# Kernel tuning notes

Hardware: AMD Instinct MI355X
Metric: run time of the kernel (lower is better)

Reference implementation:

```python
import jax, jax.numpy as jnp
import numpy as np

IN_DIM = 512
OUT_DIM = 512
KEY_DIM = 512
FILTER_LENGTH = 32
STRIDE = 4
B, T = 8, 2048


def setup_inputs() -> dict:
    key = jax.random.key(0)
    ks = jax.random.split(key, 7)
    s_in = 1.0 / np.sqrt(IN_DIM)
    x = jax.random.normal(ks[0], (B, T, IN_DIM), dtype=jnp.float32)
    Wq = jax.random.uniform(ks[1], (IN_DIM, KEY_DIM), jnp.float32, -s_in, s_in)
    bq = jax.random.uniform(ks[2], (KEY_DIM,), jnp.float32, -s_in, s_in)
    Wk = jax.random.uniform(ks[3], (IN_DIM, KEY_DIM), jnp.float32, -s_in, s_in)
    bk = jax.random.uniform(ks[4], (KEY_DIM,), jnp.float32, -s_in, s_in)
    Wv = jax.random.uniform(ks[5], (IN_DIM, OUT_DIM), jnp.float32, -s_in, s_in)
    bv = jax.random.uniform(ks[6], (OUT_DIM,), jnp.float32, -s_in, s_in)
    return {"x": x, "Wq": Wq, "bq": bq, "Wk": Wk, "bk": bk, "Wv": Wv, "bv": bv}


def reference(x, Wq, bq, Wk, bk, Wv, bv):
    # x: (B, T, in_dim)
    Bsz, T_, _ = x.shape
    F = FILTER_LENGTH
    T_out = (T_ - F) // STRIDE + 1
    starts = jnp.arange(T_out) * STRIDE                 # (T_out,)
    win_idx = starts[:, None] + jnp.arange(F)[None, :]  # (T_out, F)
    center_idx = starts + F // 2                        # (T_out,)

    q = x @ Wq + bq   # (B, T, key_dim)
    k = x @ Wk + bk   # (B, T, key_dim)
    v = x @ Wv + bv   # (B, T, out_dim)

    q_c = q[:, center_idx]    # (B, T_out, key_dim) query at window center
    k_w = k[:, win_idx]       # (B, T_out, F, key_dim)
    v_w = v[:, win_idx]       # (B, T_out, F, out_dim)

    scale = 1.0 / jnp.sqrt(jnp.asarray(KEY_DIM, dtype=q.dtype))
    scores = jnp.einsum('btd,btfd->btf', q_c, k_w) * scale  # (B, T_out, F)
    attn = jax.nn.softmax(scores, axis=-1)
    out = jnp.einsum('btf,btfd->btd', attn, v_w)            # (B, T_out, out_dim)
    return out
```

## Files before the change

### kernel.cpp

```cpp
#include <hip/hip_runtime.h>
#include <hip/hip_bf16.h>
#include <cstdint>

#define FLT 32
#define TOUT 505
#define TT 2048
#define MROWS 16384
#define QROWS 4040
#define KDIM 512
#define BK 64
#define NT 8

typedef float f32x4 __attribute__((ext_vector_type(4)));
typedef __bf16 bf16x8 __attribute__((ext_vector_type(8)));

static __device__ __forceinline__ ushort f2bf(float f) {
  uint32_t u = __float_as_uint(f);
  uint32_t r = (u + 0x7fffu + ((u >> 16) & 1u)) >> 16;
  return (ushort)r;
}
static __device__ __forceinline__ float bf2f(ushort h) {
  return __uint_as_float(((uint32_t)h) << 16);
}

__global__ void prep_kernel(const float* __restrict__ x,
                            const float* __restrict__ Wq, const float* __restrict__ Wk,
                            const float* __restrict__ Wv, const float* __restrict__ bq,
                            const float* __restrict__ bk, const float* __restrict__ bv,
                            ushort* __restrict__ xb, ushort* __restrict__ wt,
                            float* __restrict__ bias) {
  const int bid = blockIdx.x;
  const int tid = threadIdx.x;
  if (bid < 8192) {
    int i = bid * 256 + tid;
    float4 v = reinterpret_cast<const float4*>(x)[i];
    ushort4 o;
    o.x = f2bf(v.x); o.y = f2bf(v.y); o.z = f2bf(v.z); o.w = f2bf(v.w);
    reinterpret_cast<ushort4*>(xb)[i] = o;
  } else if (bid < 8384) {
    __shared__ ushort lds[64][66];
    int w = bid - 8192;
    int mat = w >> 6;
    int rem = w & 63;
    int k0 = (rem >> 3) * 64;
    int n0 = (rem & 7) * 64;
    const float* W = (mat == 0) ? Wq : (mat == 1) ? Wk : Wv;
    int nn = tid & 63;
    #pragma unroll
    for (int r = 0; r < 16; ++r) {
      int kk = r * 4 + (tid >> 6);
      lds[kk][nn] = f2bf(W[(size_t)(k0 + kk) * 512 + n0 + nn]);
    }
    __syncthreads();
    int kk2 = tid & 63;
    #pragma unroll
    for (int r = 0; r < 16; ++r) {
      int nn2 = r * 4 + (tid >> 6);
      wt[(size_t)(mat * 512 + n0 + nn2) * 512 + k0 + kk2] = lds[kk2][nn2];
    }
  } else {
    #pragma unroll
    for (int e = 0; e < 6; ++e) {
      int n = tid * 6 + e;
      const float* bsrc = (n < 512) ? bq : (n < 1024) ? bk : bv;
      bias[n] = bsrc[n & 511];
    }
  }
}

__global__ __launch_bounds__(256, 2) void gemm_kernel(
    const ushort* __restrict__ xb, const ushort* __restrict__ wt,
    const float* __restrict__ bias, ushort* __restrict__ kv, ushort* __restrict__ qc) {
  __shared__ ushort As[128 * 64];
  __shared__ ushort Bs[128 * 64];

  const int tid = threadIdx.x;
  const int lane = tid & 63;
  const int wv = tid >> 6;
  const int bid = blockIdx.x;

  int m0, n0, ost, gather;
  const ushort* wtb;
  const float* biasb;
  ushort* outp;
  if (bid < 1024) {
    int swz = (bid & 7) * 128 + (bid >> 3);
    m0 = (swz >> 3) * 128; n0 = (swz & 7) * 128;
    wtb = wt + (size_t)512 * KDIM; biasb = bias + 512;
    outp = kv; ost = 1024; gather = 0;
  } else {
    int b2 = bid - 1024;
    int swz = (b2 & 7) * 16 + (b2 >> 3);
    m0 = (swz >> 2) * 128; n0 = (swz & 3) * 128;
    wtb = wt; biasb = bias;
    outp = qc; ost = 512; gather = 1;
  }

  const ushort* aSrc[4];
  const ushort* bSrc[4];
  #pragma unroll
  for (int i = 0; i < 4; ++i) {
    int boff = i * 4096 + wv * 1024 + lane * 16;
    int row = boff >> 7;
    int colb = boff & 127;
    int scol = (colb ^ ((row & 7) << 4)) >> 1;
    size_t arow;
    if (gather) {
      int r = m0 + row;
      if (r > QROWS - 1) r = QROWS - 1;
      int bb = r / TOUT;
      int t2 = r - bb * TOUT;
      arow = (size_t)bb * TT + (size_t)t2 * 4 + FLT / 2;
    } else {
      arow = (size_t)(m0 + row);
    }
    aSrc[i] = xb + arow * KDIM + scol;
    bSrc[i] = wtb + (size_t)(n0 + row) * KDIM + scol;
  }

  const int fr = lane & 15;
  const int fq = lane >> 4;
  const int wr = wv >> 1;
  const int wc = wv & 1;

  f32x4 acc[4][4];
  #pragma unroll
  for (int i = 0; i < 4; ++i)
    #pragma unroll
    for (int j = 0; j < 4; ++j) acc[i][j] = (f32x4){0.f, 0.f, 0.f, 0.f};

  for (int t = 0; t < NT; ++t) {
    __syncthreads();
    const int koff = t * BK;
    #pragma unroll
    for (int i = 0; i < 4; ++i) {
      int ldst = i * 4096 + wv * 1024 + lane * 16;
      __builtin_amdgcn_global_load_lds(
          (const __attribute__((address_space(1))) unsigned int*)(aSrc[i] + koff),
          (__attribute__((address_space(3))) unsigned int*)((char*)As + ldst),
          16, 0, 0);
      __builtin_amdgcn_global_load_lds(
          (const __attribute__((address_space(1))) unsigned int*)(bSrc[i] + koff),
          (__attribute__((address_space(3))) unsigned int*)((char*)Bs + ldst),
          16, 0, 0);
    }
    __syncthreads();

    #pragma unroll
    for (int ks = 0; ks < 2; ++ks) {
      bf16x8 af[4], bg[4];
      #pragma unroll
      for (int i = 0; i < 4; ++i) {
        int ra = wr * 64 + i * 16 + fr;
        int ca = ks * 64 + fq * 16;
        af[i] = *reinterpret_cast<const bf16x8*>(
            (const char*)As + ra * 128 + (ca ^ ((ra & 7) << 4)));
        int rb = wc * 64 + i * 16 + fr;
        bg[i] = *reinterpret_cast<const bf16x8*>(
            (const char*)Bs + rb * 128 + (ca ^ ((rb & 7) << 4)));
      }
      #pragma unroll
      for (int i = 0; i < 4; ++i)
        #pragma unroll
        for (int j = 0; j < 4; ++j)
          acc[i][j] = __builtin_amdgcn_mfma_f32_16x16x32_bf16(af[i], bg[j], acc[i][j], 0, 0, 0);
    }
  }

  #pragma unroll
  for (int j = 0; j < 4; ++j) {
    int col = n0 + wc * 64 + j * 16 + fr;
    float bvl = biasb[col];
    #pragma unroll
    for (int i = 0; i < 4; ++i) {
      int rowb = m0 + wr * 64 + i * 16 + fq * 4;
      #pragma unroll
      for (int r = 0; r < 4; ++r) {
        if (!gather || (rowb + r) < QROWS)
          outp[(size_t)(rowb + r) * ost + col] = f2bf(acc[i][j][r] + bvl);
      }
    }
  }
}

__global__ __launch_bounds__(256) void attn_kernel(
    const ushort* __restrict__ kv,
    const ushort* __restrict__ qc,
    float* __restrict__ out) {
  __shared__ float q_lds[KDIM];
  __shared__ float s_lds[FLT];
  __shared__ float p_lds[FLT];

  const int bid = blockIdx.x;
  const int b = bid & 7;
  const int t = bid >> 3;
  const size_t base_row = (size_t)b * TT + (size_t)t * 4;
  const int tid = threadIdx.x;
  const int lane = tid & 63;
  const int wv = tid >> 6;

  {
    const ushort* qrow = qc + ((size_t)b * TOUT + t) * KDIM;
    uint v = *reinterpret_cast<const uint*>(qrow + tid * 2);
    q_lds[tid * 2]     = bf2f((ushort)(v & 0xffffu));
    q_lds[tid * 2 + 1] = bf2f((ushort)(v >> 16));
  }
  __syncthreads();

  const int fl = lane >> 3;
  const int f = wv * 8 + fl;
  const int sub = lane & 7;
  const ushort* krow = kv + (base_row + f) * 1024;
  float acc = 0.f;
  #pragma unroll
  for (int j = 0; j < 8; ++j) {
    int d = (j * 8 + sub) * 8;
    uint4 kv4 = *reinterpret_cast<const uint4*>(krow + d);
    const ushort* ks = reinterpret_cast<const ushort*>(&kv4);
    #pragma unroll
    for (int e = 0; e < 8; ++e) acc += q_lds[d + e] * bf2f(ks[e]);
  }
  acc += __shfl_xor(acc, 1);
  acc += __shfl_xor(acc, 2);
  acc += __shfl_xor(acc, 4);
  if (sub == 0) s_lds[f] = acc * 0.04419417382415922f;
  __syncthreads();

  float m = -1e30f;
  #pragma unroll
  for (int i = 0; i < FLT; ++i) m = fmaxf(m, s_lds[i]);
  if (tid < FLT) p_lds[tid] = __expf(s_lds[tid] - m);
  __syncthreads();
  float sum = 0.f;
  #pragma unroll
  for (int i = 0; i < FLT; ++i) sum += p_lds[i];
  const float inv = 1.f / sum;

  const int d = tid * 2;
  float o0 = 0.f, o1 = 0.f;
  const ushort* vbase = kv + base_row * 1024 + 512 + d;
  #pragma unroll
  for (int ff = 0; ff < FLT; ++ff) {
    uint vvv = *reinterpret_cast<const uint*>(vbase + (size_t)ff * 1024);
    float w = p_lds[ff] * inv;
    o0 += w * bf2f((ushort)(vvv & 0xffffu));
    o1 += w * bf2f((ushort)(vvv >> 16));
  }
  float2* op = reinterpret_cast<float2*>(out + ((size_t)b * TOUT + t) * 512 + d);
  *op = make_float2(o0, o1);
}

extern "C" void kernel_launch(void* const* d_in, const int* in_sizes, int n_in,
                              void* d_out, int out_size, void* d_ws, size_t ws_size,
                              hipStream_t stream) {
  const float* x  = (const float*)d_in[0];
  const float* Wq = (const float*)d_in[1];
  const float* bq = (const float*)d_in[2];
  const float* Wk = (const float*)d_in[3];
  const float* bk = (const float*)d_in[4];
  const float* Wv = (const float*)d_in[5];
  const float* bv = (const float*)d_in[6];
  float* out = (float*)d_out;

  char* ws = (char*)d_ws;
  ushort* xb   = (ushort*)ws;
  ushort* wt   = (ushort*)(ws + 16777216);
  float*  bias = (float*)(ws + 16777216 + 1572864);
  ushort* kvb  = (ushort*)(ws + 18358272);
  ushort* qc   = (ushort*)(ws + 18358272 + 33554432);

  hipLaunchKernelGGL(prep_kernel, dim3(8385), dim3(256), 0, stream,
                     x, Wq, Wk, Wv, bq, bk, bv, xb, wt, bias);
  hipLaunchKernelGGL(gemm_kernel, dim3(1152), dim3(256), 0, stream,
                     xb, wt, bias, kvb, qc);
  hipLaunchKernelGGL(attn_kernel, dim3(QROWS), dim3(256), 0, stream, kvb, qc, out);
}
```

Measured before the change: 72.13 us.

## Reassociate attention to avoid computing K and V over all timesteps

Rather than projecting K and V for every input row, the query is projected only at window centres and then multiplied by Wk (z = q·Wkᵀ), so scores become z·x over raw x windows. The key bias term is constant across a window and cancels in the softmax. The attention-weighted sum of x is then projected through Wv, and bv is added at the end because the weights sum to one. This removes the large K/V GEMM over 16384 rows, but adds two small chained GEMMs, fp32 x windows staged in LDS (64KB per block), and an extra bf16 rounding of intermediates.

```diff
diff --git a/kernel.cpp b/kernel.cpp
--- a/kernel.cpp
+++ b/kernel.cpp
@@ -2,14 +2,12 @@
 #include <hip/hip_bf16.h>
 #include <cstdint>
 
-#define FLT 32
 #define TOUT 505
-#define TT 2048
-#define MROWS 16384
+#define TT   2048
 #define QROWS 4040
-#define KDIM 512
-#define BK 64
-#define NT 8
+#define KD   512
+#define BK   128
+#define NSTEP 4
 
 typedef float f32x4 __attribute__((ext_vector_type(4)));
 typedef __bf16 bf16x8 __attribute__((ext_vector_type(8)));
@@ -23,28 +21,19 @@
   return __uint_as_float(((uint32_t)h) << 16);
 }
 
-__global__ void prep_kernel(const float* __restrict__ x,
-                            const float* __restrict__ Wq, const float* __restrict__ Wk,
-                            const float* __restrict__ Wv, const float* __restrict__ bq,
-                            const float* __restrict__ bk, const float* __restrict__ bv,
-                            ushort* __restrict__ xb, ushort* __restrict__ wt,
-                            float* __restrict__ bias) {
+__global__ void prep_kernel(const float* __restrict__ Wq, const float* __restrict__ Wk,
+                            const float* __restrict__ Wv,
+                            ushort* __restrict__ wqt, ushort* __restrict__ wvt,
+                            ushort* __restrict__ wkb) {
   const int bid = blockIdx.x;
   const int tid = threadIdx.x;
-  if (bid < 8192) {
-    int i = bid * 256 + tid;
-    float4 v = reinterpret_cast<const float4*>(x)[i];
-    ushort4 o;
-    o.x = f2bf(v.x); o.y = f2bf(v.y); o.z = f2bf(v.z); o.w = f2bf(v.w);
-    reinterpret_cast<ushort4*>(xb)[i] = o;
-  } else if (bid < 8384) {
+  if (bid < 128) {
     __shared__ ushort lds[64][66];
-    int w = bid - 8192;
-    int mat = w >> 6;
-    int rem = w & 63;
-    int k0 = (rem >> 3) * 64;
-    int n0 = (rem & 7) * 64;
-    const float* W = (mat == 0) ? Wq : (mat == 1) ? Wk : Wv;
+    int mat = bid >> 6;
+    int w = bid & 63;
+    int k0 = (w >> 3) * 64, n0 = (w & 7) * 64;
+    const float* W = mat ? Wv : Wq;
+    ushort* dst = mat ? wvt : wqt;
     int nn = tid & 63;
     #pragma unroll
     for (int r = 0; r < 16; ++r) {
@@ -56,66 +45,57 @@
     #pragma unroll
     for (int r = 0; r < 16; ++r) {
       int nn2 = r * 4 + (tid >> 6);
-      wt[(size_t)(mat * 512 + n0 + nn2) * 512 + k0 + kk2] = lds[kk2][nn2];
+      dst[(size_t)(n0 + nn2) * 512 + k0 + kk2] = lds[kk2][nn2];
     }
   } else {
-    #pragma unroll
-    for (int e = 0; e < 6; ++e) {
-      int n = tid * 6 + e;
-      const float* bsrc = (n < 512) ? bq : (n < 1024) ? bk : bv;
-      bias[n] = bsrc[n & 511];
-    }
-  }
-}
-
+    int idx = (bid - 128) * 256 + tid;
+    int e0 = idx * 8;
+    float4 a = *reinterpret_cast<const float4*>(Wk + e0);
+    float4 b = *reinterpret_cast<const float4*>(Wk + e0 + 4);
+    ushort v8[8] = {f2bf(a.x), f2bf(a.y), f2bf(a.z), f2bf(a.w),
+                    f2bf(b.x), f2bf(b.y), f2bf(b.z), f2bf(b.w)};
+    *reinterpret_cast<uint4*>(wkb + e0) = *reinterpret_cast<const uint4*>(v8);
+  }
+}
+
+template <int MODE>
 __global__ __launch_bounds__(256, 2) void gemm_kernel(
-    const ushort* __restrict__ xb, const ushort* __restrict__ wt,
-    const float* __restrict__ bias, ushort* __restrict__ kv, ushort* __restrict__ qc) {
-  __shared__ ushort As[128 * 64];
-  __shared__ ushort Bs[128 * 64];
+    const float* __restrict__ xf, const ushort* __restrict__ abuf,
+    const ushort* __restrict__ bmat, const float* __restrict__ bias,
+    ushort* __restrict__ obf, float* __restrict__ of32) {
+  __shared__ ushort As[128 * 128];
+  __shared__ ushort Bs[128 * 128];
 
   const int tid = threadIdx.x;
   const int lane = tid & 63;
   const int wv = tid >> 6;
-  const int bid = blockIdx.x;
-
-  int m0, n0, ost, gather;
-  const ushort* wtb;
-  const float* biasb;
-  ushort* outp;
-  if (bid < 1024) {
-    int swz = (bid & 7) * 128 + (bid >> 3);
-    m0 = (swz >> 3) * 128; n0 = (swz & 7) * 128;
-    wtb = wt + (size_t)512 * KDIM; biasb = bias + 512;
-    outp = kv; ost = 1024; gather = 0;
-  } else {
-    int b2 = bid - 1024;
-    int swz = (b2 & 7) * 16 + (b2 >> 3);
-    m0 = (swz >> 2) * 128; n0 = (swz & 3) * 128;
-    wtb = wt; biasb = bias;
-    outp = qc; ost = 512; gather = 1;
-  }
-
-  const ushort* aSrc[4];
-  const ushort* bSrc[4];
-  #pragma unroll
-  for (int i = 0; i < 4; ++i) {
-    int boff = i * 4096 + wv * 1024 + lane * 16;
-    int row = boff >> 7;
-    int colb = boff & 127;
-    int scol = (colb ^ ((row & 7) << 4)) >> 1;
-    size_t arow;
-    if (gather) {
-      int r = m0 + row;
-      if (r > QROWS - 1) r = QROWS - 1;
+  const int swz = (blockIdx.x & 7) * 16 + (blockIdx.x >> 3);
+  const int m0 = (swz >> 2) * 128;
+  const int n0 = (swz & 3) * 128;
+
+  const int srow = tid >> 4;
+  const int colb = (tid & 15) * 16;
+  const int scol = ((((colb & 127) ^ ((srow & 7) << 4)) + (colb & 128)) >> 1);
+
+  const ushort* bSrc[8];
+  const ushort* aSrc[8];
+  const float*  aSrcF[8];
+  uint          aDst[8];
+  #pragma unroll
+  for (int i = 0; i < 8; ++i) {
+    int row = i * 16 + srow;
+    bSrc[i] = bmat + (size_t)(n0 + row) * 512 + scol;
+    if (MODE == 0) {
+      int r = m0 + row; if (r > QROWS - 1) r = QROWS - 1;
       int bb = r / TOUT;
-      int t2 = r - bb * TOUT;
-      arow = (size_t)bb * TT + (size_t)t2 * 4 + FLT / 2;
+      int tt = r - bb * TOUT;
+      size_t arow = (size_t)bb * TT + (size_t)tt * 4 + 16;
+      aSrcF[i] = xf + arow * 512 + (colb >> 1);
+      aDst[i] = (uint)(row * 256 + (colb & 128) + ((colb & 127) ^ ((row & 7) << 4)));
     } else {
-      arow = (size_t)(m0 + row);
-    }
-    aSrc[i] = xb + arow * KDIM + scol;
-    bSrc[i] = wtb + (size_t)(n0 + row) * KDIM + scol;
+      int r = m0 + row; if (r > QROWS - 1) r = QROWS - 1;
+      aSrc[i] = abuf + (size_t)r * 512 + scol;
+    }
   }
 
   const int fr = lane & 15;
@@ -129,35 +109,44 @@
     #pragma unroll
     for (int j = 0; j < 4; ++j) acc[i][j] = (f32x4){0.f, 0.f, 0.f, 0.f};
 
-  for (int t = 0; t < NT; ++t) {
+  for (int t = 0; t < NSTEP; ++t) {
     __syncthreads();
     const int koff = t * BK;
     #pragma unroll
-    for (int i = 0; i < 4; ++i) {
-      int ldst = i * 4096 + wv * 1024 + lane * 16;
-      __builtin_amdgcn_global_load_lds(
-          (const __attribute__((address_space(1))) unsigned int*)(aSrc[i] + koff),
-          (__attribute__((address_space(3))) unsigned int*)((char*)As + ldst),
-          16, 0, 0);
+    for (int i = 0; i < 8; ++i) {
+      int ldst = i * 4096 + tid * 16;
       __builtin_amdgcn_global_load_lds(
           (const __attribute__((address_space(1))) unsigned int*)(bSrc[i] + koff),
           (__attribute__((address_space(3))) unsigned int*)((char*)Bs + ldst),
           16, 0, 0);
+      if (MODE == 0) {
+        float4 lo = *reinterpret_cast<const float4*>(aSrcF[i] + koff);
+        float4 hi = *reinterpret_cast<const float4*>(aSrcF[i] + koff + 4);
+        ushort v8[8] = {f2bf(lo.x), f2bf(lo.y), f2bf(lo.z), f2bf(lo.w),
+                        f2bf(hi.x), f2bf(hi.y), f2bf(hi.z), f2bf(hi.w)};
+        *reinterpret_cast<uint4*>((char*)As + aDst[i]) =
+            *reinterpret_cast<const uint4*>(v8);
+      } else {
+        __builtin_amdgcn_global_load_lds(
+            (const __attribute__((address_space(1))) unsigned int*)(aSrc[i] + koff),
+            (__attribute__((address_space(3))) unsigned int*)((char*)As + ldst),
+            16, 0, 0);
+      }
     }
     __syncthreads();
 
     #pragma unroll
-    for (int ks = 0; ks < 2; ++ks) {
+    for (int ks = 0; ks < 4; ++ks) {
+      const int cab = ks * 64 + fq * 16;
       bf16x8 af[4], bg[4];
       #pragma unroll
       for (int i = 0; i < 4; ++i) {
         int ra = wr * 64 + i * 16 + fr;
-        int ca = ks * 64 + fq * 16;
         af[i] = *reinterpret_cast<const bf16x8*>(
-            (const char*)As + ra * 128 + (ca ^ ((ra & 7) << 4)));
+            (const char*)As + ra * 256 + (cab & 128) + ((cab & 127) ^ ((ra & 7) << 4)));
         int rb = wc * 64 + i * 16 + fr;
         bg[i] = *reinterpret_cast<const bf16x8*>(
-            (const char*)Bs + rb * 128 + (ca ^ ((rb & 7) << 4)));
+            (const char*)Bs + rb * 256 + (cab & 128) + ((cab & 127) ^ ((rb & 7) << 4)));
       }
       #pragma unroll
       for (int i = 0; i < 4; ++i)
@@ -170,55 +159,68 @@
   #pragma unroll
   for (int j = 0; j < 4; ++j) {
     int col = n0 + wc * 64 + j * 16 + fr;
-    float bvl = biasb[col];
+    float bvl = (MODE == 1) ? 0.f : bias[col];
     #pragma unroll
     for (int i = 0; i < 4; ++i) {
       int rowb = m0 + wr * 64 + i * 16 + fq * 4;
       #pragma unroll
       for (int r = 0; r < 4; ++r) {
-        if (!gather || (rowb + r) < QROWS)
-          outp[(size_t)(rowb + r) * ost + col] = f2bf(acc[i][j][r] + bvl);
+        if (rowb + r < QROWS) {
+          float v = acc[i][j][r] + bvl;
+          if (MODE == 2) of32[(size_t)(rowb + r) * 512 + col] = v;
+          else           obf[(size_t)(rowb + r) * 512 + col] = f2bf(v);
+        }
       }
     }
   }
 }
 
 __global__ __launch_bounds__(256) void attn_kernel(
-    const ushort* __restrict__ kv,
-    const ushort* __restrict__ qc,
-    float* __restrict__ out) {
-  __shared__ float q_lds[KDIM];
-  __shared__ float s_lds[FLT];
-  __shared__ float p_lds[FLT];
+    const float* __restrict__ xf,
+    const ushort* __restrict__ zbuf,
+    ushort* __restrict__ ubuf) {
+  __shared__ float xw[32 * 512];
+  __shared__ float zl[512];
+  __shared__ float s_lds[32];
+  __shared__ float p_lds[32];
 
   const int bid = blockIdx.x;
   const int b = bid & 7;
   const int t = bid >> 3;
   const size_t base_row = (size_t)b * TT + (size_t)t * 4;
+  const int r = b * TOUT + t;
   const int tid = threadIdx.x;
   const int lane = tid & 63;
   const int wv = tid >> 6;
 
+  #pragma unroll
+  for (int i = 0; i < 16; ++i) {
+    int dst = i * 4096 + tid * 16;
+    int row = dst >> 11;
+    int cf = (dst & 2047) >> 2;
+    __builtin_amdgcn_global_load_lds(
+        (const __attribute__((address_space(1))) unsigned int*)(xf + (base_row + row) * 512 + cf),
+        (__attribute__((address_space(3))) unsigned int*)((char*)xw + dst),
+        16, 0, 0);
+  }
   {
-    const ushort* qrow = qc + ((size_t)b * TOUT + t) * KDIM;
-    uint v = *reinterpret_cast<const uint*>(qrow + tid * 2);
-    q_lds[tid * 2]     = bf2f((ushort)(v & 0xffffu));
-    q_lds[tid * 2 + 1] = bf2f((ushort)(v >> 16));
+    uint v = *reinterpret_cast<const uint*>(zbuf + (size_t)r * 512 + tid * 2);
+    zl[tid * 2]     = bf2f((ushort)(v & 0xffffu));
+    zl[tid * 2 + 1] = bf2f((ushort)(v >> 16));
   }
   __syncthreads();
 
-  const int fl = lane >> 3;
-  const int f = wv * 8 + fl;
+  const int f = wv * 8 + (lane >> 3);
   const int sub = lane & 7;
-  const ushort* krow = kv + (base_row + f) * 1024;
   float acc = 0.f;
   #pragma unroll
   for (int j = 0; j < 8; ++j) {
-    int d = (j * 8 + sub) * 8;
-    uint4 kv4 = *reinterpret_cast<const uint4*>(krow + d);
-    const ushort* ks = reinterpret_cast<const ushort*>(&kv4);
-    #pragma unroll
-    for (int e = 0; e < 8; ++e) acc += q_lds[d + e] * bf2f(ks[e]);
+    int d0 = (j * 8 + sub) * 8;
+    const float* xr = xw + f * 512 + d0;
+    float4 a = *reinterpret_cast<const float4*>(xr);
+    float4 c = *reinterpret_cast<const float4*>(xr + 4);
+    acc += zl[d0] * a.x + zl[d0 + 1] * a.y + zl[d0 + 2] * a.z + zl[d0 + 3] * a.w;
+    acc += zl[d0 + 4] * c.x + zl[d0 + 5] * c.y + zl[d0 + 6] * c.z + zl[d0 + 7] * c.w;
   }
   acc += __shfl_xor(acc, 1);
   acc += __shfl_xor(acc, 2);
@@ -228,26 +230,24 @@
 
   float m = -1e30f;
   #pragma unroll
-  for (int i = 0; i < FLT; ++i) m = fmaxf(m, s_lds[i]);
-  if (tid < FLT) p_lds[tid] = __expf(s_lds[tid] - m);
+  for (int i = 0; i < 32; ++i) m = fmaxf(m, s_lds[i]);
+  if (tid < 32) p_lds[tid] = __expf(s_lds[tid] - m);
   __syncthreads();
   float sum = 0.f;
   #pragma unroll
-  for (int i = 0; i < FLT; ++i) sum += p_lds[i];
+  for (int i = 0; i < 32; ++i) sum += p_lds[i];
   const float inv = 1.f / sum;
 
   const int d = tid * 2;
   float o0 = 0.f, o1 = 0.f;
-  const ushort* vbase = kv + base_row * 1024 + 512 + d;
-  #pragma unroll
-  for (int ff = 0; ff < FLT; ++ff) {
-    uint vvv = *reinterpret_cast<const uint*>(vbase + (size_t)ff * 1024);
+  #pragma unroll
+  for (int ff = 0; ff < 32; ++ff) {
     float w = p_lds[ff] * inv;
-    o0 += w * bf2f((ushort)(vvv & 0xffffu));
-    o1 += w * bf2f((ushort)(vvv >> 16));
-  }
-  float2* op = reinterpret_cast<float2*>(out + ((size_t)b * TOUT + t) * 512 + d);
-  *op = make_float2(o0, o1);
+    o0 += w * xw[ff * 512 + d];
+    o1 += w * xw[ff * 512 + d + 1];
+  }
+  uint pk = ((uint)f2bf(o1) << 16) | (uint)f2bf(o0);
+  *reinterpret_cast<uint*>(ubuf + (size_t)r * 512 + d) = pk;
 }
 
 extern "C" void kernel_launch(void* const* d_in, const int* in_sizes, int n_in,
@@ -257,21 +257,25 @@
   const float* Wq = (const float*)d_in[1];
   const float* bq = (const float*)d_in[2];
   const float* Wk = (const float*)d_in[3];
-  const float* bk = (const float*)d_in[4];
   const float* Wv = (const float*)d_in[5];
   const float* bv = (const float*)d_in[6];
   float* out = (float*)d_out;
 
   char* ws = (char*)d_ws;
-  ushort* xb   = (ushort*)ws;
-  ushort* wt   = (ushort*)(ws + 16777216);
-  float*  bias = (float*)(ws + 16777216 + 1572864);
-  ushort* kvb  = (ushort*)(ws + 18358272);
-  ushort* qc   = (ushort*)(ws + 18358272 + 33554432);
-
-  hipLaunchKernelGGL(prep_kernel, dim3(8385), dim3(256), 0, stream,
-                     x, Wq, Wk, Wv, bq, bk, bv, xb, wt, bias);
-  hipLaunchKernelGGL(gemm_kernel, dim3(1152), dim3(256), 0, stream,
-                     xb, wt, bias, kvb, qc);
-  hipLaunchKernelGGL(attn_kernel, dim3(QROWS), dim3(256), 0, stream, kvb, qc, out);
-}
+  ushort* wqt  = (ushort*)ws;
+  ushort* wvt  = (ushort*)(ws + 524288);
+  ushort* wkb  = (ushort*)(ws + 1048576);
+  ushort* qbuf = (ushort*)(ws + 1572864);
+  ushort* zbuf = (ushort*)(ws + 1572864 + 4194304);
+  ushort* ubuf = (ushort*)(ws + 1572864 + 8388608);
+
+  hipLaunchKernelGGL(prep_kernel, dim3(256), dim3(256), 0, stream,
+                     Wq, Wk, Wv, wqt, wvt, wkb);
+  hipLaunchKernelGGL((gemm_kernel<0>), dim3(128), dim3(256), 0, stream,
+                     x, (const ushort*)nullptr, wqt, bq, qbuf, (float*)nullptr);
+  hipLaunchKernelGGL((gemm_kernel<1>), dim3(128), dim3(256), 0, stream,
+                     (const float*)nullptr, qbuf, wkb, (const float*)nullptr, zbuf, (float*)nullptr);
+  hipLaunchKernelGGL(attn_kernel, dim3(QROWS), dim3(256), 0, stream, x, zbuf, ubuf);
+  hipLaunchKernelGGL((gemm_kernel<2>), dim3(128), dim3(256), 0, stream,
+                     (const float*)nullptr, ubuf, wvt, bv, (ushort*)nullptr, out);
+}
```

Measured after the change: 81.07 us. 12.4% more time.

## Fuse x fp32-to-bf16 conversion into GEMM loads and stage epilogue through LDS

Applied to the files above, without the earlier changes.

Removes the separate pass that converted x to bf16. The GEMM now loads fp32 x directly, converts it in registers and writes swizzled bf16 into LDS, while weights still go through direct global-to-LDS loads. The epilogue stages the output tile in LDS so it can be written with coalesced 16-byte stores. This saves a 32MB read and 16MB write round trip, but each GEMM tile now reads twice as many bytes for A through synchronous register loads that are no longer asynchronous, and the K-side tiles reread x four to eight times.

```diff
diff --git a/kernel.cpp b/kernel.cpp
--- a/kernel.cpp
+++ b/kernel.cpp
@@ -22,28 +22,22 @@
 static __device__ __forceinline__ float bf2f(ushort h) {
   return __uint_as_float(((uint32_t)h) << 16);
 }
-
-__global__ void prep_kernel(const float* __restrict__ x,
-                            const float* __restrict__ Wq, const float* __restrict__ Wk,
-                            const float* __restrict__ Wv, const float* __restrict__ bq,
-                            const float* __restrict__ bk, const float* __restrict__ bv,
-                            ushort* __restrict__ xb, ushort* __restrict__ wt,
-                            float* __restrict__ bias) {
+static __device__ __forceinline__ void pack8(const float4& lo, const float4& hi, ushort* v8) {
+  v8[0] = f2bf(lo.x); v8[1] = f2bf(lo.y); v8[2] = f2bf(lo.z); v8[3] = f2bf(lo.w);
+  v8[4] = f2bf(hi.x); v8[5] = f2bf(hi.y); v8[6] = f2bf(hi.z); v8[7] = f2bf(hi.w);
+}
+
+__global__ void wprep_kernel(const float* __restrict__ Wq, const float* __restrict__ Wk,
+                             const float* __restrict__ Wv, const float* __restrict__ bq,
+                             const float* __restrict__ bk, const float* __restrict__ bv,
+                             ushort* __restrict__ wt, float* __restrict__ bias) {
   const int bid = blockIdx.x;
   const int tid = threadIdx.x;
-  if (bid < 8192) {
-    int i = bid * 256 + tid;
-    float4 v = reinterpret_cast<const float4*>(x)[i];
-    ushort4 o;
-    o.x = f2bf(v.x); o.y = f2bf(v.y); o.z = f2bf(v.z); o.w = f2bf(v.w);
-    reinterpret_cast<ushort4*>(xb)[i] = o;
-  } else if (bid < 8384) {
+  if (bid < 192) {
     __shared__ ushort lds[64][66];
-    int w = bid - 8192;
-    int mat = w >> 6;
-    int rem = w & 63;
-    int k0 = (rem >> 3) * 64;
-    int n0 = (rem & 7) * 64;
+    int mat = bid >> 6;
+    int w = bid & 63;
+    int k0 = (w >> 3) * 64, n0 = (w & 7) * 64;
     const float* W = (mat == 0) ? Wq : (mat == 1) ? Wk : Wv;
     int nn = tid & 63;
     #pragma unroll
@@ -69,17 +63,18 @@
 }
 
 __global__ __launch_bounds__(256, 2) void gemm_kernel(
-    const ushort* __restrict__ xb, const ushort* __restrict__ wt,
+    const float* __restrict__ xf, const ushort* __restrict__ wt,
     const float* __restrict__ bias, ushort* __restrict__ kv, ushort* __restrict__ qc) {
-  __shared__ ushort As[128 * 64];
-  __shared__ ushort Bs[128 * 64];
+  __shared__ char smem[33792];
+  ushort* const As = (ushort*)smem;
+  ushort* const Bs = (ushort*)(smem + 16384);
 
   const int tid = threadIdx.x;
   const int lane = tid & 63;
   const int wv = tid >> 6;
   const int bid = blockIdx.x;
 
-  int m0, n0, ost, gather;
+  int m0, n0, ost, gather, mlim;
   const ushort* wtb;
   const float* biasb;
   ushort* outp;
@@ -87,22 +82,24 @@
     int swz = (bid & 7) * 128 + (bid >> 3);
     m0 = (swz >> 3) * 128; n0 = (swz & 7) * 128;
     wtb = wt + (size_t)512 * KDIM; biasb = bias + 512;
-    outp = kv; ost = 1024; gather = 0;
+    outp = kv; ost = 1024; gather = 0; mlim = MROWS;
   } else {
     int b2 = bid - 1024;
     int swz = (b2 & 7) * 16 + (b2 >> 3);
     m0 = (swz >> 2) * 128; n0 = (swz & 3) * 128;
     wtb = wt; biasb = bias;
-    outp = qc; ost = 512; gather = 1;
-  }
-
-  const ushort* aSrc[4];
-  const ushort* bSrc[4];
+    outp = qc; ost = 512; gather = 1; mlim = QROWS;
+  }
+
+  const float* aF[4];
+  uint aDst[4];
+  const ushort* bS[4];
   #pragma unroll
   for (int i = 0; i < 4; ++i) {
-    int boff = i * 4096 + wv * 1024 + lane * 16;
-    int row = boff >> 7;
-    int colb = boff & 127;
+    int idx = i * 4096 + tid * 16;
+    int row = idx >> 7;
+    int colb = idx & 127;
+    aDst[i] = (uint)(row * 128 + (colb ^ ((row & 7) << 4)));
     int scol = (colb ^ ((row & 7) << 4)) >> 1;
     size_t arow;
     if (gather) {
@@ -114,8 +111,8 @@
     } else {
       arow = (size_t)(m0 + row);
     }
-    aSrc[i] = xb + arow * KDIM + scol;
-    bSrc[i] = wtb + (size_t)(n0 + row) * KDIM + scol;
+    aF[i] = xf + arow * KDIM + (colb >> 1);
+    bS[i] = wtb + (size_t)(n0 + row) * KDIM + scol;
   }
 
   const int fr = lane & 15;
@@ -134,15 +131,17 @@
     const int koff = t * BK;
     #pragma unroll
     for (int i = 0; i < 4; ++i) {
-      int ldst = i * 4096 + wv * 1024 + lane * 16;
       __builtin_amdgcn_global_load_lds(
-          (const __attribute__((address_space(1))) unsigned int*)(aSrc[i] + koff),
-          (__attribute__((address_space(3))) unsigned int*)((char*)As + ldst),
+          (const __attribute__((address_space(1))) unsigned int*)(bS[i] + koff),
+          (__attribute__((address_space(3))) unsigned int*)((char*)Bs + i * 4096 + tid * 16),
           16, 0, 0);
-      __builtin_amdgcn_global_load_lds(
-          (const __attribute__((address_space(1))) unsigned int*)(bSrc[i] + koff),
-          (__attribute__((address_space(3))) unsigned int*)((char*)Bs + ldst),
-          16, 0, 0);
+    }
+    #pragma unroll
+    for (int i = 0; i < 4; ++i) {
+      float4 lo = *reinterpret_cast<const float4*>(aF[i] + koff);
+      float4 hi = *reinterpret_cast<const float4*>(aF[i] + koff + 4);
+      ushort v8[8]; pack8(lo, hi, v8);
+      *reinterpret_cast<uint4*>((char*)As + aDst[i]) = *reinterpret_cast<const uint4*>(v8);
     }
     __syncthreads();
 
@@ -167,18 +166,29 @@
     }
   }
 
+  __syncthreads();
+  ushort* const ep = (ushort*)smem;
   #pragma unroll
   for (int j = 0; j < 4; ++j) {
-    int col = n0 + wc * 64 + j * 16 + fr;
-    float bvl = biasb[col];
+    int colg = n0 + wc * 64 + j * 16 + fr;
+    int coll = wc * 64 + j * 16 + fr;
+    float bvl = biasb[colg];
     #pragma unroll
     for (int i = 0; i < 4; ++i) {
-      int rowb = m0 + wr * 64 + i * 16 + fq * 4;
+      int rowl = wr * 64 + i * 16 + fq * 4;
       #pragma unroll
-      for (int r = 0; r < 4; ++r) {
-        if (!gather || (rowb + r) < QROWS)
-          outp[(size_t)(rowb + r) * ost + col] = f2bf(acc[i][j][r] + bvl);
-      }
+      for (int r = 0; r < 4; ++r)
+        ep[(rowl + r) * 132 + coll] = f2bf(acc[i][j][r] + bvl);
+    }
+  }
+  __syncthreads();
+  #pragma unroll
+  for (int it = 0; it < 8; ++it) {
+    int row = it * 16 + (tid >> 4);
+    int gr = m0 + row;
+    if (gr < mlim) {
+      uint4 val = *reinterpret_cast<const uint4*>(&ep[row * 132 + (tid & 15) * 8]);
+      *reinterpret_cast<uint4*>(outp + (size_t)gr * ost + n0 + (tid & 15) * 8) = val;
     }
   }
 }
@@ -263,15 +273,14 @@
   float* out = (float*)d_out;
 
   char* ws = (char*)d_ws;
-  ushort* xb   = (ushort*)ws;
-  ushort* wt   = (ushort*)(ws + 16777216);
-  float*  bias = (float*)(ws + 16777216 + 1572864);
-  ushort* kvb  = (ushort*)(ws + 18358272);
-  ushort* qc   = (ushort*)(ws + 18358272 + 33554432);
-
-  hipLaunchKernelGGL(prep_kernel, dim3(8385), dim3(256), 0, stream,
-                     x, Wq, Wk, Wv, bq, bk, bv, xb, wt, bias);
+  ushort* wt   = (ushort*)ws;
+  float*  bias = (float*)(ws + 1572864);
+  ushort* kvb  = (ushort*)(ws + 1581056);
+  ushort* qc   = (ushort*)(ws + 1581056 + 33554432);
+
+  hipLaunchKernelGGL(wprep_kernel, dim3(193), dim3(256), 0, stream,
+                     Wq, Wk, Wv, bq, bk, bv, wt, bias);
   hipLaunchKernelGGL(gemm_kernel, dim3(1152), dim3(256), 0, stream,
-                     xb, wt, bias, kvb, qc);
+                     x, wt, bias, kvb, qc);
   hipLaunchKernelGGL(attn_kernel, dim3(QROWS), dim3(256), 0, stream, kvb, qc, out);
 }
```

New measurement: 60.25 us, median of 3. -16.5%, faster.
